# Performance work log

Measured on AMD Instinct MI355X. Metric: run time of the kernel, lower is better.

The kernel has to match this reference:

```python
import jax, jax.numpy as jnp
import numpy as np

CUBIC_A = -0.75  # torch bicubic kernel coefficient


def _cubic(d):
    a = CUBIC_A
    ad = jnp.abs(d)
    near = (a + 2.0) * ad**3 - (a + 3.0) * ad**2 + 1.0
    far = a * (ad**3 - 5.0 * ad**2 + 8.0 * ad - 4.0)
    return jnp.where(ad <= 1.0, near, jnp.where(ad < 2.0, far, 0.0))


def _axis_weights(in_size, out_size):
    # half-pixel centers (align_corners=False), 4-tap cubic, edge clamp (matches torch)
    scale = in_size / out_size
    src = (jnp.arange(out_size, dtype=jnp.float32) + 0.5) * scale - 0.5
    i0 = jnp.floor(src).astype(jnp.int32)
    offs = jnp.arange(-1, 3)
    taps = i0[:, None] + offs[None, :]          # (out, 4)
    idx = jnp.clip(taps, 0, in_size - 1)
    w = _cubic(src[:, None] - taps.astype(jnp.float32))
    return idx, w


def _bicubic(img, h, w):
    # img: (H, W, C) -> (h, w, C), separable bicubic
    H, W, _ = img.shape
    ih, wh = _axis_weights(H, h)
    iw, ww = _axis_weights(W, w)
    rows = jnp.einsum('ot,otwc->owc', wh, img[ih])   # (h, W, C)
    out = jnp.einsum('ot,hotc->hoc', ww, rows[:, iw])  # (h, w, C)
    return out


def _sincos_1d(embed_dim, t_size):
    omega = np.arange(embed_dim // 2, dtype=np.float32) / (embed_dim / 2.0)
    omega = 1.0 / 10000 ** omega
    out = np.einsum('m,d->md', np.arange(t_size, dtype=np.float32), omega)
    return np.concatenate([np.sin(out), np.cos(out)], axis=1)


HEIGHT, WIDTH, NUM_FRAMES, DIM = 64, 64, 16, 1024
GRIDS = [(8, 32, 32), (8, 48, 48), (4, 64, 64), (1, 64, 64)]


def setup_inputs() -> dict:
    key = jax.random.key(0)
    k1, k2 = jax.random.split(key)
    total = sum(t * h * w for t, h, w in GRIDS)  # 47104
    x = jax.random.normal(k1, (total, DIM), dtype=jnp.float32)
    weight = jax.random.normal(k2, (HEIGHT, WIDTH, DIM), dtype=jnp.float32) * 0.02
    time_weight = jnp.asarray(_sincos_1d(DIM, NUM_FRAMES))[:, None, :]  # (T, 1, dim)
    grid_thws = jnp.asarray(GRIDS, dtype=jnp.int64)
    return {"x": x, "weight": weight, "time_weight": time_weight, "grid_thws": grid_thws}


def reference(x, weight, time_weight, grid_thws):
    H, W, dim = weight.shape
    grids = np.asarray(grid_thws).tolist()  # static per-sample shapes
    pos_embs = []
    for t, h, w in grids:
        if (h, w) == (H, W):
            pe2 = weight.reshape(-1, dim)
        else:
            pe2 = _bicubic(weight, h, w).reshape(-1, dim)
        if t == 1:
            pe3 = pe2
        else:
            pe3 = pe2[None, :, :] + time_weight[:t]  # (t, h*w, dim)
        pos_embs.append(pe3.reshape(-1, dim))
    return x + jnp.concatenate(pos_embs, axis=0)
```

## Files before the change

kernel.cpp:

```cpp
#include <hip/hip_runtime.h>

#define CUBIC_A (-0.75f)

typedef float f4nt __attribute__((ext_vector_type(4)));

__device__ __forceinline__ void nt_store4(float4* p, float4 v) {
    f4nt t;
    t.x = v.x; t.y = v.y; t.z = v.z; t.w = v.w;
    __builtin_nontemporal_store(t, (f4nt*)p);
}

__device__ __forceinline__ float cubic_w(float d) {
    float ad = fabsf(d);
    if (ad <= 1.0f) return ((CUBIC_A + 2.0f) * ad - (CUBIC_A + 3.0f)) * ad * ad + 1.0f;
    if (ad < 2.0f)  return CUBIC_A * (((ad - 5.0f) * ad + 8.0f) * ad - 4.0f);
    return 0.0f;
}

template <int T>
__device__ __forceinline__ void add_frames(const float4* __restrict__ x,
                                           const float4* __restrict__ tw,
                                           float4* __restrict__ out,
                                           size_t rowbase, int ppf, int px, int d4,
                                           float4 pe) {
    const size_t base = (rowbase + (size_t)px) * 256 + d4;
    const size_t fstride = (size_t)ppf * 256;
    float4 xv[T];
#pragma unroll
    for (int f = 0; f < T; ++f) xv[f] = x[base + (size_t)f * fstride];
    if (T > 1) {
        float4 tv[T];
#pragma unroll
        for (int f = 0; f < T; ++f) tv[f] = tw[(size_t)f * 256 + d4];
#pragma unroll
        for (int f = 0; f < T; ++f) {
            nt_store4(&out[base + (size_t)f * fstride],
                      make_float4(xv[f].x + pe.x + tv[f].x,
                                  xv[f].y + pe.y + tv[f].y,
                                  xv[f].z + pe.z + tv[f].z,
                                  xv[f].w + pe.w + tv[f].w));
        }
    } else {
        nt_store4(&out[base],
                  make_float4(xv[0].x + pe.x, xv[0].y + pe.y,
                              xv[0].z + pe.z, xv[0].w + pe.w));
    }
}

__device__ __forceinline__ float4 bicubic_pe(const float4* __restrict__ wgt,
                                             int px, int out_hw, int d4) {
    const int i = px / out_hw;
    const int j = px % out_hw;
    const float scale = 64.0f / (float)out_hw;
    const float si = ((float)i + 0.5f) * scale - 0.5f;
    const float sj = ((float)j + 0.5f) * scale - 0.5f;
    const int i0 = (int)floorf(si);
    const int j0 = (int)floorf(sj);
    int ih[4], iw[4];
    float wh[4], ww[4];
#pragma unroll
    for (int a = 0; a < 4; ++a) {
        int tp = i0 - 1 + a;
        wh[a] = cubic_w(si - (float)tp);
        ih[a] = min(63, max(0, tp));
        tp = j0 - 1 + a;
        ww[a] = cubic_w(sj - (float)tp);
        iw[a] = min(63, max(0, tp));
    }
    float ax = 0.f, ay = 0.f, az = 0.f, aw = 0.f;
#pragma unroll
    for (int a = 0; a < 4; ++a) {
        float rx = 0.f, ry = 0.f, rz = 0.f, rw = 0.f;
#pragma unroll
        for (int c = 0; c < 4; ++c) {
            const float4 v = wgt[(size_t)(ih[a] * 64 + iw[c]) * 256 + d4];
            rx = fmaf(ww[c], v.x, rx);
            ry = fmaf(ww[c], v.y, ry);
            rz = fmaf(ww[c], v.z, rz);
            rw = fmaf(ww[c], v.w, rw);
        }
        ax = fmaf(wh[a], rx, ax);
        ay = fmaf(wh[a], ry, ay);
        az = fmaf(wh[a], rz, az);
        aw = fmaf(wh[a], rw, aw);
    }
    return make_float4(ax, ay, az, aw);
}

__global__ __launch_bounds__(256) void posemb_add_kernel(
    const float4* __restrict__ x,
    const float4* __restrict__ wgt,
    const float4* __restrict__ tw,
    float4* __restrict__ out)
{
    const int b  = blockIdx.x;
    const int d4 = threadIdx.x;

    if (b < 1024) {
        const int px = b;
        const float4 pe = bicubic_pe(wgt, px, 32, d4);
        add_frames<8>(x, tw, out, 0, 1024, px, d4, pe);
    } else if (b < 3328) {
        const int px = b - 1024;
        const float4 pe = bicubic_pe(wgt, px, 48, d4);
        add_frames<8>(x, tw, out, 8192, 2304, px, d4, pe);
    } else if (b < 7424) {
        const int px = b - 3328;
        const float4 pe = wgt[(size_t)px * 256 + d4];
        add_frames<4>(x, tw, out, 26624, 4096, px, d4, pe);
    } else {
        const int px = b - 7424;
        const float4 pe = wgt[(size_t)px * 256 + d4];
        add_frames<1>(x, tw, out, 43008, 4096, px, d4, pe);
    }
}

extern "C" void kernel_launch(void* const* d_in, const int* in_sizes, int n_in,
                              void* d_out, int out_size, void* d_ws, size_t ws_size,
                              hipStream_t stream) {
    const float4* x   = (const float4*)d_in[0];
    const float4* wgt = (const float4*)d_in[1];
    const float4* tw  = (const float4*)d_in[2];
    float4* out = (float4*)d_out;
    posemb_add_kernel<<<11520, 256, 0, stream>>>(x, wgt, tw, out);
}
```

Measured before the change: 78.25 us.

## Split frames across two thread halves with 512-thread blocks

Blocks now have 512 threads, and the two 256-thread halves each take alternate frames of the same pixel. For the bicubic grids each thread now holds 4 frames instead of 8, which lowers register pressure and the serial chain of loads. The bicubic interpolation is recomputed by both halves, so the gather from weight is done twice as often per pixel. The final t=1 grid packs two pixels per block, and the grid shrinks from 11520 to 9472 blocks.

Result: no change. 76.72 us (-2.0%).

```diff
diff --git a/kernel.cpp b/kernel.cpp
--- a/kernel.cpp
+++ b/kernel.cpp
@@ -10,41 +10,19 @@
     __builtin_nontemporal_store(t, (f4nt*)p);
 }
 
+__device__ __forceinline__ float4 add3(float4 a, float4 b, float4 c) {
+    return make_float4(a.x + b.x + c.x, a.y + b.y + c.y,
+                       a.z + b.z + c.z, a.w + b.w + c.w);
+}
+__device__ __forceinline__ float4 add2(float4 a, float4 b) {
+    return make_float4(a.x + b.x, a.y + b.y, a.z + b.z, a.w + b.w);
+}
+
 __device__ __forceinline__ float cubic_w(float d) {
     float ad = fabsf(d);
     if (ad <= 1.0f) return ((CUBIC_A + 2.0f) * ad - (CUBIC_A + 3.0f)) * ad * ad + 1.0f;
     if (ad < 2.0f)  return CUBIC_A * (((ad - 5.0f) * ad + 8.0f) * ad - 4.0f);
     return 0.0f;
-}
-
-template <int T>
-__device__ __forceinline__ void add_frames(const float4* __restrict__ x,
-                                           const float4* __restrict__ tw,
-                                           float4* __restrict__ out,
-                                           size_t rowbase, int ppf, int px, int d4,
-                                           float4 pe) {
-    const size_t base = (rowbase + (size_t)px) * 256 + d4;
-    const size_t fstride = (size_t)ppf * 256;
-    float4 xv[T];
-#pragma unroll
-    for (int f = 0; f < T; ++f) xv[f] = x[base + (size_t)f * fstride];
-    if (T > 1) {
-        float4 tv[T];
-#pragma unroll
-        for (int f = 0; f < T; ++f) tv[f] = tw[(size_t)f * 256 + d4];
-#pragma unroll
-        for (int f = 0; f < T; ++f) {
-            nt_store4(&out[base + (size_t)f * fstride],
-                      make_float4(xv[f].x + pe.x + tv[f].x,
-                                  xv[f].y + pe.y + tv[f].y,
-                                  xv[f].z + pe.z + tv[f].z,
-                                  xv[f].w + pe.w + tv[f].w));
-        }
-    } else {
-        nt_store4(&out[base],
-                  make_float4(xv[0].x + pe.x, xv[0].y + pe.y,
-                              xv[0].z + pe.z, xv[0].w + pe.w));
-    }
 }
 
 __device__ __forceinline__ float4 bicubic_pe(const float4* __restrict__ wgt,
@@ -87,31 +65,68 @@
     return make_float4(ax, ay, az, aw);
 }
 
-__global__ __launch_bounds__(256) void posemb_add_kernel(
+__global__ __launch_bounds__(512) void posemb_kernel(
     const float4* __restrict__ x,
     const float4* __restrict__ wgt,
     const float4* __restrict__ tw,
     float4* __restrict__ out)
 {
-    const int b  = blockIdx.x;
-    const int d4 = threadIdx.x;
+    const int b   = blockIdx.x;
+    const int tid = threadIdx.x;
+    const int d4  = tid & 255;
+    const int fh  = tid >> 8;
 
     if (b < 1024) {
         const int px = b;
+        const size_t base = ((size_t)(fh * 1024 + px)) * 256 + d4;
+        const size_t st   = (size_t)2048 * 256;
+        const float4 xv0 = x[base];
+        const float4 xv1 = x[base + st];
+        const float4 xv2 = x[base + 2 * st];
+        const float4 xv3 = x[base + 3 * st];
+        const float4 tv0 = tw[(size_t)(fh    ) * 256 + d4];
+        const float4 tv1 = tw[(size_t)(fh + 2) * 256 + d4];
+        const float4 tv2 = tw[(size_t)(fh + 4) * 256 + d4];
+        const float4 tv3 = tw[(size_t)(fh + 6) * 256 + d4];
         const float4 pe = bicubic_pe(wgt, px, 32, d4);
-        add_frames<8>(x, tw, out, 0, 1024, px, d4, pe);
+        nt_store4(&out[base],          add3(xv0, pe, tv0));
+        nt_store4(&out[base + st],     add3(xv1, pe, tv1));
+        nt_store4(&out[base + 2 * st], add3(xv2, pe, tv2));
+        nt_store4(&out[base + 3 * st], add3(xv3, pe, tv3));
     } else if (b < 3328) {
         const int px = b - 1024;
+        const size_t base = ((size_t)(8192 + fh * 2304 + px)) * 256 + d4;
+        const size_t st   = (size_t)2 * 2304 * 256;
+        const float4 xv0 = x[base];
+        const float4 xv1 = x[base + st];
+        const float4 xv2 = x[base + 2 * st];
+        const float4 xv3 = x[base + 3 * st];
+        const float4 tv0 = tw[(size_t)(fh    ) * 256 + d4];
+        const float4 tv1 = tw[(size_t)(fh + 2) * 256 + d4];
+        const float4 tv2 = tw[(size_t)(fh + 4) * 256 + d4];
+        const float4 tv3 = tw[(size_t)(fh + 6) * 256 + d4];
         const float4 pe = bicubic_pe(wgt, px, 48, d4);
-        add_frames<8>(x, tw, out, 8192, 2304, px, d4, pe);
+        nt_store4(&out[base],          add3(xv0, pe, tv0));
+        nt_store4(&out[base + st],     add3(xv1, pe, tv1));
+        nt_store4(&out[base + 2 * st], add3(xv2, pe, tv2));
+        nt_store4(&out[base + 3 * st], add3(xv3, pe, tv3));
     } else if (b < 7424) {
         const int px = b - 3328;
+        const size_t base = ((size_t)(26624 + fh * 4096 + px)) * 256 + d4;
+        const size_t st   = (size_t)2 * 4096 * 256;
+        const float4 xv0 = x[base];
+        const float4 xv1 = x[base + st];
+        const float4 pe  = wgt[(size_t)px * 256 + d4];
+        const float4 tv0 = tw[(size_t)(fh    ) * 256 + d4];
+        const float4 tv1 = tw[(size_t)(fh + 2) * 256 + d4];
+        nt_store4(&out[base],      add3(xv0, pe, tv0));
+        nt_store4(&out[base + st], add3(xv1, pe, tv1));
+    } else {
+        const int px = 2 * (b - 7424) + fh;
+        const size_t e = ((size_t)(43008 + px)) * 256 + d4;
+        const float4 xv = x[e];
         const float4 pe = wgt[(size_t)px * 256 + d4];
-        add_frames<4>(x, tw, out, 26624, 4096, px, d4, pe);
-    } else {
-        const int px = b - 7424;
-        const float4 pe = wgt[(size_t)px * 256 + d4];
-        add_frames<1>(x, tw, out, 43008, 4096, px, d4, pe);
+        nt_store4(&out[e], add2(xv, pe));
     }
 }
 
@@ -122,5 +137,5 @@
     const float4* wgt = (const float4*)d_in[1];
     const float4* tw  = (const float4*)d_in[2];
     float4* out = (float4*)d_out;
-    posemb_add_kernel<<<11520, 256, 0, stream>>>(x, wgt, tw, out);
+    posemb_kernel<<<9472, 512, 0, stream>>>(x, wgt, tw, out);
 }
```
